# Kernel tuning notes

Hardware: AMD Instinct MI355X
Metric: run time of the kernel (lower is better)

Reference implementation:

```python
import jax, jax.numpy as jnp
import numpy as np

TOP_K = 2          # n_activated_experts
ROUTE_SCALE = 1.0  # args.route_scale


def setup_inputs() -> dict:
    key = jax.random.key(0)
    ks = jax.random.split(key, 12)
    B, S, D, I, E = 8, 2048, 512, 1024, 8
    SH = 2 * I  # n_shared_experts * moe_inter_dim
    std = 0.02
    return {
        "x": jax.random.normal(ks[0], (B, S, D), jnp.float32),
        "gate_w": (jax.random.normal(ks[1], (E, D), jnp.float32) * std),
        "w1": (jax.random.normal(ks[2], (E, D, I), jnp.float32) * std),
        "w2": (jax.random.normal(ks[3], (E, I, D), jnp.float32) * std),
        "w3": (jax.random.normal(ks[4], (E, D, I), jnp.float32) * std),
        "sw1": (jax.random.normal(ks[5], (D, SH), jnp.float32) * std),
        "sb1": jnp.zeros((SH,), jnp.float32),
        "sw2": (jax.random.normal(ks[6], (SH, D), jnp.float32) * std),
        "sb2": jnp.zeros((D,), jnp.float32),
        "sw3": (jax.random.normal(ks[7], (D, SH), jnp.float32) * std),
        "sb3": jnp.zeros((SH,), jnp.float32),
    }


def reference(x, gate_w, w1, w2, w3, sw1, sb1, sw2, sb2, sw3, sb3):
    B, S, D = x.shape
    xt = x.reshape(-1, D)              # [T, D] tokens
    T = xt.shape[0]
    E = gate_w.shape[0]

    # --- Gate: sigmoid scores, top-k, renormalized weights ---
    scores = jax.nn.sigmoid(xt @ gate_w.T)                 # [T, E]
    topv, topi = jax.lax.top_k(scores, TOP_K)              # [T, K]
    wts = topv / jnp.sum(topv, axis=-1, keepdims=True)
    wts = wts * ROUTE_SCALE

    # Dense combine weights: zero for non-selected experts -> faithful to
    # the torch masked scatter-accumulate over the expert loop.
    cw = jnp.zeros((T, E), xt.dtype).at[jnp.arange(T)[:, None], topi].add(wts)

    # --- Routed SwiGLU experts (ffn_bias=False) ---
    y = jnp.zeros_like(xt)
    for e in range(E):  # fixed small structural loop over experts
        h = jax.nn.silu(xt @ w1[e]) * (xt @ w3[e])         # [T, I]
        y = y + cw[:, e:e + 1] * (h @ w2[e])               # combine

    # --- Load-balance aux loss L_ExpBal ---
    counts = jnp.zeros((E,), xt.dtype).at[topi.reshape(-1)].add(1.0)
    f_i = E * counts / (TOP_K * T)
    P_i = cw.sum(axis=0) / T   # per-expert sum of routed weights
    L_ExpBal = jnp.sum(f_i * P_i)

    # --- Shared experts MLP (biased Linear, SwiGLU) ---
    z = (jax.nn.silu(xt @ sw1 + sb1) * (xt @ sw3 + sb3)) @ sw2 + sb2

    return (y + z).reshape(B, S, D), L_ExpBal
```

## Files before the change

kernel.cpp:

```cpp
#include <hip/hip_runtime.h>
#include <math.h>
#include <stdint.h>

#define T_TOK 16384
#define DDIM  512
#define IDIM  1024
#define NEXP  8
#define SHDIM 2048
#define MT_R  264
#define MPAD  (MT_R * 128)
#define GBLK  256

typedef unsigned short u16;
typedef short bf16x8 __attribute__((ext_vector_type(8)));
typedef float f32x4 __attribute__((ext_vector_type(4)));

__device__ __forceinline__ u16 f2bf(float f) {
    unsigned u = __float_as_uint(f);
    u += 0x7FFF + ((u >> 16) & 1);
    return (u16)(u >> 16);
}
__device__ __forceinline__ float bf2f(u16 h) {
    return __uint_as_float((unsigned)h << 16);
}

__device__ __forceinline__ void gload_lds16(const void* g, void* l) {
    __builtin_amdgcn_global_load_lds(
        (const __attribute__((address_space(1))) void*)g,
        (__attribute__((address_space(3))) void*)l, 16, 0, 0);
}

__device__ __forceinline__ int xcd_swz(int id, int nwg) {
    return (id & 7) * (nwg >> 3) + (id >> 3);
}

__device__ __forceinline__ int ksw(int r) { return (r >> 1) & 3; }

__global__ void k_zero(int* cursors) {
    int i = threadIdx.x;
    if (i < NEXP) cursors[i] = 0;
}

__global__ __launch_bounds__(256) void k_gate(
    const float* __restrict__ x, const float* __restrict__ gw,
    int* __restrict__ topi, float* __restrict__ wts,
    int* __restrict__ pcnt, float* __restrict__ pps, u16* __restrict__ xb)
{
    __shared__ int   cnt[NEXP];
    __shared__ float ps[NEXP];
    const int tid = threadIdx.x;
    if (tid < NEXP) { cnt[tid] = 0; ps[tid] = 0.f; }
    __syncthreads();
    const int wid = tid >> 6, lane = tid & 63;

    const float4* gw4 = (const float4*)gw;
    float4 g0[NEXP], g1[NEXP];
#pragma unroll
    for (int e = 0; e < NEXP; e++) {
        g0[e] = gw4[e * 128 + lane];
        g1[e] = gw4[e * 128 + 64 + lane];
    }

    const int t0 = blockIdx.x * 64 + wid * 16;
    for (int u = 0; u < 16; u++) {
        int t = t0 + u;
        const float4* xr4 = (const float4*)(x + (size_t)t * DDIM);
        float4 v0 = xr4[lane];
        float4 v1 = xr4[64 + lane];
        ushort4 o0 = { f2bf(v0.x), f2bf(v0.y), f2bf(v0.z), f2bf(v0.w) };
        ushort4 o1 = { f2bf(v1.x), f2bf(v1.y), f2bf(v1.z), f2bf(v1.w) };
        ushort4* xbo = (ushort4*)(xb + (size_t)t * DDIM);
        xbo[lane] = o0;
        xbo[64 + lane] = o1;
        float acc[NEXP];
#pragma unroll
        for (int e = 0; e < NEXP; e++) {
            acc[e] = v0.x * g0[e].x + v0.y * g0[e].y + v0.z * g0[e].z + v0.w * g0[e].w
                   + v1.x * g1[e].x + v1.y * g1[e].y + v1.z * g1[e].z + v1.w * g1[e].w;
        }
#pragma unroll
        for (int e = 0; e < NEXP; e++) {
#pragma unroll
            for (int off = 32; off; off >>= 1) acc[e] += __shfl_xor(acc[e], off, 64);
        }
        if (lane == 0) {
            float s[NEXP];
#pragma unroll
            for (int e = 0; e < NEXP; e++) s[e] = 1.f / (1.f + expf(-acc[e]));
            int i1 = 0; float v1s = s[0];
#pragma unroll
            for (int e = 1; e < NEXP; e++) if (s[e] > v1s) { v1s = s[e]; i1 = e; }
            int i2 = -1; float v2s = -1.f;
#pragma unroll
            for (int e = 0; e < NEXP; e++) if (e != i1 && s[e] > v2s) { v2s = s[e]; i2 = e; }
            float inv = 1.f / (v1s + v2s);
            float wa = v1s * inv, wb = v2s * inv;
            topi[2 * t] = i1; topi[2 * t + 1] = i2;
            wts[2 * t] = wa;  wts[2 * t + 1] = wb;
            atomicAdd(&cnt[i1], 1); atomicAdd(&cnt[i2], 1);
            atomicAdd(&ps[i1], wa); atomicAdd(&ps[i2], wb);
        }
    }
    __syncthreads();
    if (tid < NEXP) {
        pcnt[blockIdx.x * NEXP + tid] = cnt[tid];
        pps[blockIdx.x * NEXP + tid]  = ps[tid];
    }
}

__global__ void k_scan(const int* __restrict__ pcnt, const float* __restrict__ pps,
                       int* __restrict__ off_pad, float* __restrict__ out_loss)
{
    __shared__ int   scnt[8][NEXP];
    __shared__ float sps[8][NEXP];
    int tid = threadIdx.x;
    if (tid < 64) {
        int e = tid & 7, part = tid >> 3;
        int c = 0; float p = 0.f;
        for (int b = part * 32; b < part * 32 + 32; b++) {
            c += pcnt[b * NEXP + e];
            p += pps[b * NEXP + e];
        }
        scnt[part][e] = c; sps[part][e] = p;
    }
    __syncthreads();
    if (tid == 0) {
        int off = 0; float L = 0.f;
        for (int e = 0; e < NEXP; e++) {
            int c = 0; float p = 0.f;
            for (int q = 0; q < 8; q++) { c += scnt[q][e]; p += sps[q][e]; }
            off_pad[e] = off;
            off += (c + 127) & ~127;
            float f = (float)NEXP * (float)c / (float)(2 * T_TOK);
            L += f * (p / (float)T_TOK);
        }
        off_pad[NEXP] = off;
        out_loss[0] = L;
    }
}

__global__ void k_fillperm(int* __restrict__ perm, u16* __restrict__ zpad) {
    int i = blockIdx.x * blockDim.x + threadIdx.x;
    if (i < MPAD) perm[i] = -1;
    if (blockIdx.x == 0 && threadIdx.x < 256) ((unsigned*)zpad)[threadIdx.x] = 0u;
}

__global__ __launch_bounds__(256) void k_scatter(
    const int* __restrict__ topi, const float* __restrict__ wts,
    const int* __restrict__ off_pad, int* __restrict__ cursors,
    int* __restrict__ perm, float* __restrict__ pw, int* __restrict__ inv)
{
    __shared__ int lcnt[NEXP];
    __shared__ int lbase[NEXP];
    int tid = threadIdx.x;
    if (tid < NEXP) lcnt[tid] = 0;
    __syncthreads();
    int t = blockIdx.x * 256 + tid;
    int e0 = topi[2 * t], e1 = topi[2 * t + 1];
    int p0 = atomicAdd(&lcnt[e0], 1);
    int p1 = atomicAdd(&lcnt[e1], 1);
    __syncthreads();
    if (tid < NEXP) lbase[tid] = atomicAdd(&cursors[tid], lcnt[tid]);
    __syncthreads();
    int s0 = off_pad[e0] + lbase[e0] + p0;
    int s1 = off_pad[e1] + lbase[e1] + p1;
    perm[s0] = t; pw[s0] = wts[2 * t];
    perm[s1] = t; pw[s1] = wts[2 * t + 1];
    inv[2 * t] = s0; inv[2 * t + 1] = s1;
}

__global__ __launch_bounds__(256) void k_transpose(const float* __restrict__ src,
                                                   u16* __restrict__ dst, int R, int C)
{
    __shared__ u16 t[64][68];
    const float* s = src + (size_t)blockIdx.z * R * C;
    u16* d = dst + (size_t)blockIdx.z * R * C;
    int r0 = blockIdx.y * 64, c0 = blockIdx.x * 64;
    int tid = threadIdx.x;
    int lr = tid >> 4, lc = (tid & 15) * 4;
#pragma unroll
    for (int u = 0; u < 4; u++) {
        int r = lr + u * 16;
        float4 v = *(const float4*)&s[(size_t)(r0 + r) * C + c0 + lc];
        t[lc + 0][r] = f2bf(v.x);
        t[lc + 1][r] = f2bf(v.y);
        t[lc + 2][r] = f2bf(v.z);
        t[lc + 3][r] = f2bf(v.w);
    }
    __syncthreads();
    int wr = tid >> 4, wc = (tid & 15) * 4;
#pragma unroll
    for (int u = 0; u < 4; u++) {
        int c = wr + u * 16;
        ushort4 o = { t[c][wc], t[c][wc + 1], t[c][wc + 2], t[c][wc + 3] };
        *(ushort4*)&d[(size_t)(c0 + c) * R + r0 + wc] = o;
    }
}

template<bool ROUTED, bool BIAS>
__global__ __launch_bounds__(256, 3) void k_s1(
    const u16* __restrict__ Axb, const u16* __restrict__ B1t, const u16* __restrict__ B3t,
    const float* __restrict__ bias1, const float* __restrict__ bias3,
    u16* __restrict__ H, int ldh, const int* __restrict__ off_pad,
    const int* __restrict__ perm, const u16* __restrict__ zpad)
{
    __shared__ __align__(16) unsigned char smem[3 * 16384];
    const int nwg = gridDim.x * gridDim.y;
    const int id  = xcd_swz(blockIdx.y * gridDim.x + blockIdx.x, nwg);
    const int m0 = (id / gridDim.x) * 128;
    const int n0 = (id % gridDim.x) * 64;
    if (ROUTED && m0 >= off_pad[NEXP]) return;
    const u16* b1 = B1t; const u16* b3 = B3t;
    if (ROUTED) {
        int e = 0;
        while (off_pad[e + 1] <= m0) e++;
        b1 += (size_t)e * IDIM * DDIM;
        b3 += (size_t)e * IDIM * DDIM;
    }
    const int tid = threadIdx.x;
    const int wid = tid >> 6, lane = tid & 63;
    const int fr = lane & 15, hi = lane >> 4;
    const int wrow = (wid >> 1) * 64, wcol = (wid & 1) * 32;

    const u16* ap[2]; const u16* b1p; const u16* b3p;
    int dstA[2];
#pragma unroll
    for (int s = 0; s < 2; s++) {
        int r = s * 64 + (tid >> 2);
        int goff = ((tid & 3) ^ ksw(r)) * 8;
        dstA[s] = s * 4096 + tid * 16;
        if (ROUTED) {
            int tok = perm[m0 + r];
            ap[s] = (tok >= 0 ? Axb + (size_t)tok * DDIM : zpad) + goff;
        } else {
            ap[s] = Axb + (size_t)(m0 + r) * DDIM + goff;
        }
    }
    {
        int rb = tid >> 2;
        int goffb = ((tid & 3) ^ ksw(rb)) * 8;
        b1p = b1 + (size_t)(n0 + rb) * DDIM + goffb;
        b3p = b3 + (size_t)(n0 + rb) * DDIM + goffb;
    }
    const int dstB = tid * 16;

    int aoff[4], boff[2];
#pragma unroll
    for (int i = 0; i < 4; i++) {
        int ar = wrow + i * 16 + fr;
        aoff[i] = ar * 64 + ((hi ^ ksw(ar)) << 4);
    }
#pragma unroll
    for (int j = 0; j < 2; j++) {
        int br = wcol + j * 16 + fr;
        boff[j] = br * 64 + ((hi ^ ksw(br)) << 4);
    }

    f32x4 acc1[4][2], acc3[4][2];
#pragma unroll
    for (int i = 0; i < 4; i++)
#pragma unroll
        for (int j = 0; j < 2; j++) { acc1[i][j] = {0.f, 0.f, 0.f, 0.f}; acc3[i][j] = {0.f, 0.f, 0.f, 0.f}; }

    const int NT = DDIM / 32;
#pragma unroll
    for (int t = 0; t < 2; t++) {
        unsigned char* bb = smem + t * 16384;
        gload_lds16(ap[0] + t * 32, bb + dstA[0]);
        gload_lds16(ap[1] + t * 32, bb + dstA[1]);
        gload_lds16(b1p   + t * 32, bb + 8192  + dstB);
        gload_lds16(b3p   + t * 32, bb + 12288 + dstB);
    }

    int bufc = 0;
    for (int t = 0; t < NT; t++) {
        int bufn = bufc + 2; if (bufn >= 3) bufn -= 3;
        if (t + 2 < NT) {
            unsigned char* bb = smem + bufn * 16384;
            int k2 = (t + 2) * 32;
            gload_lds16(ap[0] + k2, bb + dstA[0]);
            gload_lds16(ap[1] + k2, bb + dstA[1]);
            gload_lds16(b1p   + k2, bb + 8192  + dstB);
            gload_lds16(b3p   + k2, bb + 12288 + dstB);
            asm volatile("s_waitcnt vmcnt(8)" ::: "memory");
        } else if (t + 2 == NT) {
            asm volatile("s_waitcnt vmcnt(4)" ::: "memory");
        } else {
            asm volatile("s_waitcnt vmcnt(0)" ::: "memory");
        }
        __builtin_amdgcn_s_barrier();
        __builtin_amdgcn_sched_barrier(0);
        const unsigned char* cb = smem + bufc * 16384;
        bf16x8 av[4], b1v[2], b3v[2];
#pragma unroll
        for (int i = 0; i < 4; i++) av[i] = *(const bf16x8*)(cb + aoff[i]);
#pragma unroll
        for (int j = 0; j < 2; j++) {
            b1v[j] = *(const bf16x8*)(cb + 8192  + boff[j]);
            b3v[j] = *(const bf16x8*)(cb + 12288 + boff[j]);
        }
        __builtin_amdgcn_s_setprio(1);
#pragma unroll
        for (int i = 0; i < 4; i++)
#pragma unroll
            for (int j = 0; j < 2; j++) {
                acc1[i][j] = __builtin_amdgcn_mfma_f32_16x16x32_bf16(av[i], b1v[j], acc1[i][j], 0, 0, 0);
                acc3[i][j] = __builtin_amdgcn_mfma_f32_16x16x32_bf16(av[i], b3v[j], acc3[i][j], 0, 0, 0);
            }
        __builtin_amdgcn_s_setprio(0);
        __builtin_amdgcn_sched_barrier(0);
        __builtin_amdgcn_s_barrier();
        bufc++; if (bufc >= 3) bufc -= 3;
    }

    const int rr = hi * 4;
#pragma unroll
    for (int i = 0; i < 4; i++) {
#pragma unroll
        for (int j = 0; j < 2; j++) {
            int col = n0 + wcol + j * 16 + fr;
            float bb1 = BIAS ? bias1[col] : 0.f;
            float bb3 = BIAS ? bias3[col] : 0.f;
#pragma unroll
            for (int r = 0; r < 4; r++) {
                int row = m0 + wrow + i * 16 + rr + r;
                float v1 = acc1[i][j][r] + bb1;
                float v3 = acc3[i][j][r] + bb3;
                float hv = (v1 / (1.f + __expf(-v1))) * v3;
                H[(size_t)row * ldh + col] = f2bf(hv);
            }
        }
    }
}

template<int K, bool ROUTED>
__global__ __launch_bounds__(256, 3) void k_s2(
    const u16* __restrict__ A, const u16* __restrict__ Bt,
    const float* __restrict__ bias2, float* __restrict__ out,
    u16* __restrict__ ytmp, const int* __restrict__ off_pad)
{
    __shared__ __align__(16) unsigned char smem[3 * 16384];
    const int nwg = gridDim.x * gridDim.y;
    const int id  = xcd_swz(blockIdx.y * gridDim.x + blockIdx.x, nwg);
    const int m0 = (id / gridDim.x) * 128;
    const int n0 = (id % gridDim.x) * 128;
    if (ROUTED && m0 >= off_pad[NEXP]) return;
    const u16* bt = Bt;
    if (ROUTED) {
        int e = 0;
        while (off_pad[e + 1] <= m0) e++;
        bt += (size_t)e * DDIM * IDIM;
    }
    const int tid = threadIdx.x;
    const int wid = tid >> 6, lane = tid & 63;
    const int fr = lane & 15, hi = lane >> 4;
    const int wrow = (wid >> 1) * 64, wcol = (wid & 1) * 64;

    const u16* ap[2]; const u16* bp[2];
    int dst_[2];
#pragma unroll
    for (int s = 0; s < 2; s++) {
        int r = s * 64 + (tid >> 2);
        int goff = ((tid & 3) ^ ksw(r)) * 8;
        dst_[s] = s * 4096 + tid * 16;
        ap[s] = A  + (size_t)(m0 + r) * K + goff;
        bp[s] = bt + (size_t)(n0 + r) * K + goff;
    }
    int aoff[4], boff[4];
#pragma unroll
    for (int i = 0; i < 4; i++) {
        int ar = wrow + i * 16 + fr;
        aoff[i] = ar * 64 + ((hi ^ ksw(ar)) << 4);
        int br = wcol + i * 16 + fr;
        boff[i] = br * 64 + ((hi ^ ksw(br)) << 4);
    }

    f32x4 acc[4][4];
#pragma unroll
    for (int i = 0; i < 4; i++)
#pragma unroll
        for (int j = 0; j < 4; j++) acc[i][j] = {0.f, 0.f, 0.f, 0.f};

    const int NT = K / 32;
#pragma unroll
    for (int t = 0; t < 2; t++) {
        unsigned char* bb = smem + t * 16384;
#pragma unroll
        for (int s = 0; s < 2; s++) {
            gload_lds16(ap[s] + t * 32, bb + dst_[s]);
            gload_lds16(bp[s] + t * 32, bb + 8192 + dst_[s]);
        }
    }

    int bufc = 0;
    for (int t = 0; t < NT; t++) {
        int bufn = bufc + 2; if (bufn >= 3) bufn -= 3;
        if (t + 2 < NT) {
            unsigned char* bb = smem + bufn * 16384;
            int k2 = (t + 2) * 32;
#pragma unroll
            for (int s = 0; s < 2; s++) {
                gload_lds16(ap[s] + k2, bb + dst_[s]);
                gload_lds16(bp[s] + k2, bb + 8192 + dst_[s]);
            }
            asm volatile("s_waitcnt vmcnt(8)" ::: "memory");
        } else if (t + 2 == NT) {
            asm volatile("s_waitcnt vmcnt(4)" ::: "memory");
        } else {
            asm volatile("s_waitcnt vmcnt(0)" ::: "memory");
        }
        __builtin_amdgcn_s_barrier();
        __builtin_amdgcn_sched_barrier(0);
        const unsigned char* cb = smem + bufc * 16384;
        bf16x8 av[4], bv[4];
#pragma unroll
        for (int i = 0; i < 4; i++) {
            av[i] = *(const bf16x8*)(cb + aoff[i]);
            bv[i] = *(const bf16x8*)(cb + 8192 + boff[i]);
        }
        __builtin_amdgcn_s_setprio(1);
#pragma unroll
        for (int i = 0; i < 4; i++)
#pragma unroll
            for (int j = 0; j < 4; j++)
                acc[i][j] = __builtin_amdgcn_mfma_f32_16x16x32_bf16(av[i], bv[j], acc[i][j], 0, 0, 0);
        __builtin_amdgcn_s_setprio(0);
        __builtin_amdgcn_sched_barrier(0);
        __builtin_amdgcn_s_barrier();
        bufc++; if (bufc >= 3) bufc -= 3;
    }

    const int rr = hi * 4;
#pragma unroll
    for (int i = 0; i < 4; i++) {
#pragma unroll
        for (int r = 0; r < 4; r++) {
            int row = m0 + wrow + i * 16 + rr + r;
#pragma unroll
            for (int j = 0; j < 4; j++) {
                int col = n0 + wcol + j * 16 + fr;
                float v = acc[i][j][r];
                if (ROUTED) {
                    ytmp[(size_t)row * DDIM + col] = f2bf(v);
                } else {
                    out[(size_t)row * DDIM + col] = v + bias2[col];
                }
            }
        }
    }
}

__global__ __launch_bounds__(256) void k_combine(
    const u16* __restrict__ ytmp, const int* __restrict__ inv,
    const float* __restrict__ wts, float* __restrict__ out)
{
    int idx = blockIdx.x * 256 + threadIdx.x;
    int t = idx >> 7;
    int c = (idx & 127) * 4;
    int s0 = inv[2 * t], s1 = inv[2 * t + 1];
    float w0 = wts[2 * t], w1 = wts[2 * t + 1];
    ushort4 a = *(const ushort4*)&ytmp[(size_t)s0 * DDIM + c];
    ushort4 b = *(const ushort4*)&ytmp[(size_t)s1 * DDIM + c];
    float4 o = *(float4*)&out[(size_t)t * DDIM + c];
    o.x += w0 * bf2f(a.x) + w1 * bf2f(b.x);
    o.y += w0 * bf2f(a.y) + w1 * bf2f(b.y);
    o.z += w0 * bf2f(a.z) + w1 * bf2f(b.z);
    o.w += w0 * bf2f(a.w) + w1 * bf2f(b.w);
    *(float4*)&out[(size_t)t * DDIM + c] = o;
}

extern "C" void kernel_launch(void* const* d_in, const int* in_sizes, int n_in,
                              void* d_out, int out_size, void* d_ws, size_t ws_size,
                              hipStream_t stream)
{
    const float* x   = (const float*)d_in[0];
    const float* gw  = (const float*)d_in[1];
    const float* w1  = (const float*)d_in[2];
    const float* w2  = (const float*)d_in[3];
    const float* w3  = (const float*)d_in[4];
    const float* sw1 = (const float*)d_in[5];
    const float* sb1 = (const float*)d_in[6];
    const float* sw2 = (const float*)d_in[7];
    const float* sb2 = (const float*)d_in[8];
    const float* sw3 = (const float*)d_in[9];
    const float* sb3 = (const float*)d_in[10];
    float* out = (float*)d_out;

    char* ws = (char*)d_ws;
    size_t off = 0;
    int*   topi    = (int*)(ws + off);   off += (size_t)2 * T_TOK * 4;
    float* wts     = (float*)(ws + off); off += (size_t)2 * T_TOK * 4;
    int*   perm    = (int*)(ws + off);   off += (size_t)MPAD * 4;
    float* pw      = (float*)(ws + off); off += (size_t)MPAD * 4;
    int*   cursors = (int*)(ws + off);   off += 256;
    int*   off_pad = (int*)(ws + off);   off += 256;
    int*   pcnt    = (int*)(ws + off);   off += (size_t)GBLK * NEXP * 4;
    float* pps     = (float*)(ws + off); off += (size_t)GBLK * NEXP * 4;
    int*   inv     = (int*)(ws + off);   off += (size_t)2 * T_TOK * 4;
    u16*   zpad    = (u16*)(ws + off);   off += 1024;
    u16*   xb      = (u16*)(ws + off);   off += (size_t)T_TOK * DDIM * 2;
    u16*   ytmp    = (u16*)(ws + off);   off += (size_t)MPAD * DDIM * 2;
    u16*   w1T     = (u16*)(ws + off);   off += (size_t)NEXP * IDIM * DDIM * 2;
    u16*   w3T     = (u16*)(ws + off);   off += (size_t)NEXP * IDIM * DDIM * 2;
    u16*   w2T     = (u16*)(ws + off);   off += (size_t)NEXP * DDIM * IDIM * 2;
    u16*   sw1T    = (u16*)(ws + off);   off += (size_t)SHDIM * DDIM * 2;
    u16*   sw3T    = (u16*)(ws + off);   off += (size_t)SHDIM * DDIM * 2;
    u16*   sw2T    = (u16*)(ws + off);   off += (size_t)DDIM * SHDIM * 2;
    u16*   hb      = (u16*)(ws + off);   off += (size_t)MPAD * IDIM * 2;

    k_zero<<<1, 64, 0, stream>>>(cursors);
    k_gate<<<GBLK, 256, 0, stream>>>(x, gw, topi, wts, pcnt, pps, xb);
    k_scan<<<1, 64, 0, stream>>>(pcnt, pps, off_pad, out + (size_t)T_TOK * DDIM);
    k_fillperm<<<MPAD / 256, 256, 0, stream>>>(perm, zpad);
    k_scatter<<<T_TOK / 256, 256, 0, stream>>>(topi, wts, off_pad, cursors, perm, pw, inv);

    k_transpose<<<dim3(IDIM / 64, DDIM / 64, NEXP), 256, 0, stream>>>(w1, w1T, DDIM, IDIM);
    k_transpose<<<dim3(IDIM / 64, DDIM / 64, NEXP), 256, 0, stream>>>(w3, w3T, DDIM, IDIM);
    k_transpose<<<dim3(DDIM / 64, IDIM / 64, NEXP), 256, 0, stream>>>(w2, w2T, IDIM, DDIM);
    k_transpose<<<dim3(SHDIM / 64, DDIM / 64, 1), 256, 0, stream>>>(sw1, sw1T, DDIM, SHDIM);
    k_transpose<<<dim3(SHDIM / 64, DDIM / 64, 1), 256, 0, stream>>>(sw3, sw3T, DDIM, SHDIM);
    k_transpose<<<dim3(DDIM / 64, SHDIM / 64, 1), 256, 0, stream>>>(sw2, sw2T, SHDIM, DDIM);

    k_s1<false, true><<<dim3(SHDIM / 64, T_TOK / 128), 256, 0, stream>>>(
        xb, sw1T, sw3T, sb1, sb3, hb, SHDIM, nullptr, nullptr, nullptr);
    k_s2<SHDIM, false><<<dim3(DDIM / 128, T_TOK / 128), 256, 0, stream>>>(
        hb, sw2T, sb2, out, nullptr, nullptr);
    k_s1<true, false><<<dim3(IDIM / 64, MT_R), 256, 0, stream>>>(
        xb, w1T, w3T, nullptr, nullptr, hb, IDIM, off_pad, perm, zpad);
    k_s2<IDIM, true><<<dim3(DDIM / 128, MT_R), 256, 0, stream>>>(
        hb, w2T, nullptr, nullptr, ytmp, off_pad);
    k_combine<<<(T_TOK * DDIM / 4) / 256, 256, 0, stream>>>(ytmp, inv, wts, out);
}
```

Baseline: 355.8 us.

## Make GEMM kernels persistent with cross-tile prefetch and per-XCD job partitioning

Converts the four GEMM kernels from one-tile-per-block grids to persistent kernels with a fixed grid of 768 blocks. Each XCD gets a contiguous range of tile jobs, and the first k-slices of the next tile are prefetched into LDS while the current tile finishes. For the routed experts, only the tiles that are actually populated are distributed, instead of launching the padded maximum and early-exiting. A separate zero-init kernel launch is also folded into the scan kernel. The cost is extra register pressure and more control logic in the main loop.

```diff
diff --git a/kernel.cpp b/kernel.cpp
--- a/kernel.cpp
+++ b/kernel.cpp
@@ -10,6 +10,8 @@
 #define MT_R  264
 #define MPAD  (MT_R * 128)
 #define GBLK  256
+#define NB    768
+#define BPX   96
 
 typedef unsigned short u16;
 typedef short bf16x8 __attribute__((ext_vector_type(8)));
@@ -30,16 +32,7 @@
         (__attribute__((address_space(3))) void*)l, 16, 0, 0);
 }
 
-__device__ __forceinline__ int xcd_swz(int id, int nwg) {
-    return (id & 7) * (nwg >> 3) + (id >> 3);
-}
-
 __device__ __forceinline__ int ksw(int r) { return (r >> 1) & 3; }
-
-__global__ void k_zero(int* cursors) {
-    int i = threadIdx.x;
-    if (i < NEXP) cursors[i] = 0;
-}
 
 __global__ __launch_bounds__(256) void k_gate(
     const float* __restrict__ x, const float* __restrict__ gw,
@@ -109,11 +102,13 @@
 }
 
 __global__ void k_scan(const int* __restrict__ pcnt, const float* __restrict__ pps,
-                       int* __restrict__ off_pad, float* __restrict__ out_loss)
+                       int* __restrict__ off_pad, float* __restrict__ out_loss,
+                       int* __restrict__ cursors)
 {
     __shared__ int   scnt[8][NEXP];
     __shared__ float sps[8][NEXP];
     int tid = threadIdx.x;
+    if (tid < NEXP) cursors[tid] = 0;
     if (tid < 64) {
         int e = tid & 7, part = tid >> 3;
         int c = 0; float p = 0.f;
@@ -197,52 +192,59 @@
     }
 }
 
-template<bool ROUTED, bool BIAS>
+struct S1Src { const u16 *a0, *a1, *b1, *b3; int m0, n0; };
+struct S2Src { const u16 *a0, *a1, *b0, *b1; int m0, n0; };
+
+template<bool ROUTED>
+__device__ __forceinline__ S1Src s1_build(
+    int m0, int n0, int tk0, int tk1, int r0, int g0,
+    const u16* Axb, const u16* B1t, const u16* B3t,
+    const int* opad, const u16* zpad)
+{
+    S1Src s; s.m0 = m0; s.n0 = n0;
+    const u16* b1 = B1t; const u16* b3 = B3t;
+    if (ROUTED) {
+        int e = 0;
+#pragma unroll
+        for (int k = 1; k < NEXP; k++) e += (opad[k] <= m0) ? 1 : 0;
+        b1 += (size_t)e * IDIM * DDIM;
+        b3 += (size_t)e * IDIM * DDIM;
+        s.a0 = (tk0 >= 0 ? Axb + (size_t)tk0 * DDIM : zpad) + g0;
+        s.a1 = (tk1 >= 0 ? Axb + (size_t)tk1 * DDIM : zpad) + g0;
+    } else {
+        s.a0 = Axb + (size_t)(m0 + r0) * DDIM + g0;
+        s.a1 = Axb + (size_t)(m0 + 64 + r0) * DDIM + g0;
+    }
+    s.b1 = b1 + (size_t)(n0 + r0) * DDIM + g0;
+    s.b3 = b3 + (size_t)(n0 + r0) * DDIM + g0;
+    return s;
+}
+
+template<bool ROUTED, bool BIAS, int GX>
 __global__ __launch_bounds__(256, 3) void k_s1(
     const u16* __restrict__ Axb, const u16* __restrict__ B1t, const u16* __restrict__ B3t,
     const float* __restrict__ bias1, const float* __restrict__ bias3,
     u16* __restrict__ H, int ldh, const int* __restrict__ off_pad,
-    const int* __restrict__ perm, const u16* __restrict__ zpad)
+    const int* __restrict__ perm, const u16* __restrict__ zpad, int njobs_s)
 {
     __shared__ __align__(16) unsigned char smem[3 * 16384];
-    const int nwg = gridDim.x * gridDim.y;
-    const int id  = xcd_swz(blockIdx.y * gridDim.x + blockIdx.x, nwg);
-    const int m0 = (id / gridDim.x) * 128;
-    const int n0 = (id % gridDim.x) * 64;
-    if (ROUTED && m0 >= off_pad[NEXP]) return;
-    const u16* b1 = B1t; const u16* b3 = B3t;
-    if (ROUTED) {
-        int e = 0;
-        while (off_pad[e + 1] <= m0) e++;
-        b1 += (size_t)e * IDIM * DDIM;
-        b3 += (size_t)e * IDIM * DDIM;
-    }
+    int opad[NEXP + 1];
+#pragma unroll
+    for (int k = 0; k <= NEXP; k++) opad[k] = ROUTED ? off_pad[k] : 0;
+    const int njobs = ROUTED ? ((opad[NEXP] >> 7) * GX) : njobs_s;
+    const int b = blockIdx.x, xcd = b & 7, bx = b >> 3;
+    const int q = njobs >> 3, r8 = njobs & 7;
+    const int base = xcd < r8 ? xcd * (q + 1) : r8 * (q + 1) + (xcd - r8) * q;
+    const int cnt = q + (xcd < r8 ? 1 : 0);
+    if (bx >= cnt) return;
+
     const int tid = threadIdx.x;
     const int wid = tid >> 6, lane = tid & 63;
     const int fr = lane & 15, hi = lane >> 4;
     const int wrow = (wid >> 1) * 64, wcol = (wid & 1) * 32;
-
-    const u16* ap[2]; const u16* b1p; const u16* b3p;
-    int dstA[2];
-#pragma unroll
-    for (int s = 0; s < 2; s++) {
-        int r = s * 64 + (tid >> 2);
-        int goff = ((tid & 3) ^ ksw(r)) * 8;
-        dstA[s] = s * 4096 + tid * 16;
-        if (ROUTED) {
-            int tok = perm[m0 + r];
-            ap[s] = (tok >= 0 ? Axb + (size_t)tok * DDIM : zpad) + goff;
-        } else {
-            ap[s] = Axb + (size_t)(m0 + r) * DDIM + goff;
-        }
-    }
-    {
-        int rb = tid >> 2;
-        int goffb = ((tid & 3) ^ ksw(rb)) * 8;
-        b1p = b1 + (size_t)(n0 + rb) * DDIM + goffb;
-        b3p = b3 + (size_t)(n0 + rb) * DDIM + goffb;
-    }
-    const int dstB = tid * 16;
+    const int r0 = tid >> 2;
+    const int g0 = ((tid & 3) ^ ksw(r0)) * 8;
+    const int dstT = tid * 16;
 
     int aoff[4], boff[2];
 #pragma unroll
@@ -256,6 +258,13 @@
         boff[j] = br * 64 + ((hi ^ ksw(br)) << 4);
     }
 
+#define S1_STAGE(S, kk, bb) do { \
+        gload_lds16((S).a0 + (kk), (bb) + dstT); \
+        gload_lds16((S).a1 + (kk), (bb) + 4096 + dstT); \
+        gload_lds16((S).b1 + (kk), (bb) + 8192 + dstT); \
+        gload_lds16((S).b3 + (kk), (bb) + 12288 + dstT); \
+    } while (0)
+
     f32x4 acc1[4][2], acc3[4][2];
 #pragma unroll
     for (int i = 0; i < 4; i++)
@@ -263,109 +272,122 @@
         for (int j = 0; j < 2; j++) { acc1[i][j] = {0.f, 0.f, 0.f, 0.f}; acc3[i][j] = {0.f, 0.f, 0.f, 0.f}; }
 
     const int NT = DDIM / 32;
-#pragma unroll
-    for (int t = 0; t < 2; t++) {
-        unsigned char* bb = smem + t * 16384;
-        gload_lds16(ap[0] + t * 32, bb + dstA[0]);
-        gload_lds16(ap[1] + t * 32, bb + dstA[1]);
-        gload_lds16(b1p   + t * 32, bb + 8192  + dstB);
-        gload_lds16(b3p   + t * 32, bb + 12288 + dstB);
-    }
+
+    int lj = bx;
+    int j0 = base + lj;
+    int m0c = (j0 / GX) * 128, n0c = (j0 % GX) * 64;
+    int tk0 = 0, tk1 = 0;
+    if (ROUTED) { tk0 = perm[m0c + r0]; tk1 = perm[m0c + 64 + r0]; }
+    S1Src cur = s1_build<ROUTED>(m0c, n0c, tk0, tk1, r0, g0, Axb, B1t, B3t, opad, zpad);
+    S1_STAGE(cur, 0, smem);
+    S1_STAGE(cur, 32, smem + 16384);
 
     int bufc = 0;
-    for (int t = 0; t < NT; t++) {
-        int bufn = bufc + 2; if (bufn >= 3) bufn -= 3;
-        if (t + 2 < NT) {
+    while (true) {
+        const bool hn = (lj + BPX) < cnt;
+        int m0n = 0, n0n = 0, ntk0 = 0, ntk1 = 0;
+        if (hn) {
+            int jn = base + lj + BPX;
+            m0n = (jn / GX) * 128; n0n = (jn % GX) * 64;
+            if (ROUTED) { ntk0 = perm[m0n + r0]; ntk1 = perm[m0n + 64 + r0]; }
+        }
+        S1Src nxt;
+        for (int t = 0; t < NT; t++) {
+            int bufn = bufc + 2; if (bufn >= 3) bufn -= 3;
             unsigned char* bb = smem + bufn * 16384;
-            int k2 = (t + 2) * 32;
-            gload_lds16(ap[0] + k2, bb + dstA[0]);
-            gload_lds16(ap[1] + k2, bb + dstA[1]);
-            gload_lds16(b1p   + k2, bb + 8192  + dstB);
-            gload_lds16(b3p   + k2, bb + 12288 + dstB);
-            asm volatile("s_waitcnt vmcnt(8)" ::: "memory");
-        } else if (t + 2 == NT) {
-            asm volatile("s_waitcnt vmcnt(4)" ::: "memory");
-        } else {
-            asm volatile("s_waitcnt vmcnt(0)" ::: "memory");
-        }
-        __builtin_amdgcn_s_barrier();
-        __builtin_amdgcn_sched_barrier(0);
-        const unsigned char* cb = smem + bufc * 16384;
-        bf16x8 av[4], b1v[2], b3v[2];
-#pragma unroll
-        for (int i = 0; i < 4; i++) av[i] = *(const bf16x8*)(cb + aoff[i]);
-#pragma unroll
-        for (int j = 0; j < 2; j++) {
-            b1v[j] = *(const bf16x8*)(cb + 8192  + boff[j]);
-            b3v[j] = *(const bf16x8*)(cb + 12288 + boff[j]);
-        }
-        __builtin_amdgcn_s_setprio(1);
+            if (t + 2 < NT) {
+                S1_STAGE(cur, (t + 2) * 32, bb);
+                asm volatile("s_waitcnt vmcnt(8)" ::: "memory");
+            } else if (hn) {
+                if (t + 2 == NT)
+                    nxt = s1_build<ROUTED>(m0n, n0n, ntk0, ntk1, r0, g0, Axb, B1t, B3t, opad, zpad);
+                S1_STAGE(nxt, (t + 2 - NT) * 32, bb);
+                asm volatile("s_waitcnt vmcnt(8)" ::: "memory");
+            } else if (t + 2 == NT) {
+                asm volatile("s_waitcnt vmcnt(4)" ::: "memory");
+            } else {
+                asm volatile("s_waitcnt vmcnt(0)" ::: "memory");
+            }
+            __builtin_amdgcn_s_barrier();
+            __builtin_amdgcn_sched_barrier(0);
+            const unsigned char* cb = smem + bufc * 16384;
+            bf16x8 av[4], b1v[2], b3v[2];
+#pragma unroll
+            for (int i = 0; i < 4; i++) av[i] = *(const bf16x8*)(cb + aoff[i]);
+#pragma unroll
+            for (int j = 0; j < 2; j++) {
+                b1v[j] = *(const bf16x8*)(cb + 8192  + boff[j]);
+                b3v[j] = *(const bf16x8*)(cb + 12288 + boff[j]);
+            }
+            __builtin_amdgcn_s_setprio(1);
+#pragma unroll
+            for (int i = 0; i < 4; i++)
+#pragma unroll
+                for (int j = 0; j < 2; j++) {
+                    acc1[i][j] = __builtin_amdgcn_mfma_f32_16x16x32_bf16(av[i], b1v[j], acc1[i][j], 0, 0, 0);
+                    acc3[i][j] = __builtin_amdgcn_mfma_f32_16x16x32_bf16(av[i], b3v[j], acc3[i][j], 0, 0, 0);
+                }
+            __builtin_amdgcn_s_setprio(0);
+            __builtin_amdgcn_sched_barrier(0);
+            __builtin_amdgcn_s_barrier();
+            bufc++; if (bufc >= 3) bufc -= 3;
+        }
+
+        const int rr = hi * 4;
+#pragma unroll
+        for (int i = 0; i < 4; i++) {
+#pragma unroll
+            for (int j = 0; j < 2; j++) {
+                int col = cur.n0 + wcol + j * 16 + fr;
+                float bb1 = BIAS ? bias1[col] : 0.f;
+                float bb3 = BIAS ? bias3[col] : 0.f;
+#pragma unroll
+                for (int r = 0; r < 4; r++) {
+                    int row = cur.m0 + wrow + i * 16 + rr + r;
+                    float v1 = acc1[i][j][r] + bb1;
+                    float v3 = acc3[i][j][r] + bb3;
+                    float hv = (v1 / (1.f + __expf(-v1))) * v3;
+                    H[(size_t)row * ldh + col] = f2bf(hv);
+                }
+            }
+        }
+        if (!hn) break;
 #pragma unroll
         for (int i = 0; i < 4; i++)
 #pragma unroll
-            for (int j = 0; j < 2; j++) {
-                acc1[i][j] = __builtin_amdgcn_mfma_f32_16x16x32_bf16(av[i], b1v[j], acc1[i][j], 0, 0, 0);
-                acc3[i][j] = __builtin_amdgcn_mfma_f32_16x16x32_bf16(av[i], b3v[j], acc3[i][j], 0, 0, 0);
-            }
-        __builtin_amdgcn_s_setprio(0);
-        __builtin_amdgcn_sched_barrier(0);
-        __builtin_amdgcn_s_barrier();
-        bufc++; if (bufc >= 3) bufc -= 3;
-    }
-
-    const int rr = hi * 4;
-#pragma unroll
-    for (int i = 0; i < 4; i++) {
-#pragma unroll
-        for (int j = 0; j < 2; j++) {
-            int col = n0 + wcol + j * 16 + fr;
-            float bb1 = BIAS ? bias1[col] : 0.f;
-            float bb3 = BIAS ? bias3[col] : 0.f;
-#pragma unroll
-            for (int r = 0; r < 4; r++) {
-                int row = m0 + wrow + i * 16 + rr + r;
-                float v1 = acc1[i][j][r] + bb1;
-                float v3 = acc3[i][j][r] + bb3;
-                float hv = (v1 / (1.f + __expf(-v1))) * v3;
-                H[(size_t)row * ldh + col] = f2bf(hv);
-            }
-        }
-    }
-}
-
-template<int K, bool ROUTED>
+            for (int j = 0; j < 2; j++) { acc1[i][j] = {0.f, 0.f, 0.f, 0.f}; acc3[i][j] = {0.f, 0.f, 0.f, 0.f}; }
+        cur = nxt;
+        lj += BPX;
+    }
+#undef S1_STAGE
+}
+
+template<int K, int EPI, int GX>
 __global__ __launch_bounds__(256, 3) void k_s2(
     const u16* __restrict__ A, const u16* __restrict__ Bt,
     const float* __restrict__ bias2, float* __restrict__ out,
-    u16* __restrict__ ytmp, const int* __restrict__ off_pad)
-{
+    u16* __restrict__ ytmp, const int* __restrict__ off_pad, int njobs_s)
+{
+    constexpr bool ROUTED = (EPI == 2);
     __shared__ __align__(16) unsigned char smem[3 * 16384];
-    const int nwg = gridDim.x * gridDim.y;
-    const int id  = xcd_swz(blockIdx.y * gridDim.x + blockIdx.x, nwg);
-    const int m0 = (id / gridDim.x) * 128;
-    const int n0 = (id % gridDim.x) * 128;
-    if (ROUTED && m0 >= off_pad[NEXP]) return;
-    const u16* bt = Bt;
-    if (ROUTED) {
-        int e = 0;
-        while (off_pad[e + 1] <= m0) e++;
-        bt += (size_t)e * DDIM * IDIM;
-    }
+    int opad[NEXP + 1];
+#pragma unroll
+    for (int k = 0; k <= NEXP; k++) opad[k] = ROUTED ? off_pad[k] : 0;
+    const int njobs = ROUTED ? ((opad[NEXP] >> 7) * GX) : njobs_s;
+    const int b = blockIdx.x, xcd = b & 7, bx = b >> 3;
+    const int q = njobs >> 3, r8 = njobs & 7;
+    const int base = xcd < r8 ? xcd * (q + 1) : r8 * (q + 1) + (xcd - r8) * q;
+    const int cnt = q + (xcd < r8 ? 1 : 0);
+    if (bx >= cnt) return;
+
     const int tid = threadIdx.x;
     const int wid = tid >> 6, lane = tid & 63;
     const int fr = lane & 15, hi = lane >> 4;
     const int wrow = (wid >> 1) * 64, wcol = (wid & 1) * 64;
-
-    const u16* ap[2]; const u16* bp[2];
-    int dst_[2];
-#pragma unroll
-    for (int s = 0; s < 2; s++) {
-        int r = s * 64 + (tid >> 2);
-        int goff = ((tid & 3) ^ ksw(r)) * 8;
-        dst_[s] = s * 4096 + tid * 16;
-        ap[s] = A  + (size_t)(m0 + r) * K + goff;
-        bp[s] = bt + (size_t)(n0 + r) * K + goff;
-    }
+    const int r0 = tid >> 2;
+    const int g0 = ((tid & 3) ^ ksw(r0)) * 8;
+    const int dstT = tid * 16;
+
     int aoff[4], boff[4];
 #pragma unroll
     for (int i = 0; i < 4; i++) {
@@ -375,6 +397,29 @@
         boff[i] = br * 64 + ((hi ^ ksw(br)) << 4);
     }
 
+    auto build = [&](int m0, int n0) {
+        S2Src s; s.m0 = m0; s.n0 = n0;
+        const u16* bt = Bt;
+        if (ROUTED) {
+            int e = 0;
+#pragma unroll
+            for (int k = 1; k < NEXP; k++) e += (opad[k] <= m0) ? 1 : 0;
+            bt += (size_t)e * DDIM * IDIM;
+        }
+        s.a0 = A  + (size_t)(m0 + r0) * K + g0;
+        s.a1 = A  + (size_t)(m0 + 64 + r0) * K + g0;
+        s.b0 = bt + (size_t)(n0 + r0) * K + g0;
+        s.b1 = bt + (size_t)(n0 + 64 + r0) * K + g0;
+        return s;
+    };
+
+#define S2_STAGE(S, kk, bb) do { \
+        gload_lds16((S).a0 + (kk), (bb) + dstT); \
+        gload_lds16((S).a1 + (kk), (bb) + 4096 + dstT); \
+        gload_lds16((S).b0 + (kk), (bb) + 8192 + dstT); \
+        gload_lds16((S).b1 + (kk), (bb) + 12288 + dstT); \
+    } while (0)
+
     f32x4 acc[4][4];
 #pragma unroll
     for (int i = 0; i < 4; i++)
@@ -382,72 +427,82 @@
         for (int j = 0; j < 4; j++) acc[i][j] = {0.f, 0.f, 0.f, 0.f};
 
     const int NT = K / 32;
-#pragma unroll
-    for (int t = 0; t < 2; t++) {
-        unsigned char* bb = smem + t * 16384;
-#pragma unroll
-        for (int s = 0; s < 2; s++) {
-            gload_lds16(ap[s] + t * 32, bb + dst_[s]);
-            gload_lds16(bp[s] + t * 32, bb + 8192 + dst_[s]);
-        }
-    }
+
+    int lj = bx;
+    int j0 = base + lj;
+    S2Src cur = build((j0 / GX) * 128, (j0 % GX) * 128);
+    S2_STAGE(cur, 0, smem);
+    S2_STAGE(cur, 32, smem + 16384);
 
     int bufc = 0;
-    for (int t = 0; t < NT; t++) {
-        int bufn = bufc + 2; if (bufn >= 3) bufn -= 3;
-        if (t + 2 < NT) {
+    while (true) {
+        const bool hn = (lj + BPX) < cnt;
+        int m0n = 0, n0n = 0;
+        if (hn) {
+            int jn = base + lj + BPX;
+            m0n = (jn / GX) * 128; n0n = (jn % GX) * 128;
+        }
+        S2Src nxt;
+        for (int t = 0; t < NT; t++) {
+            int bufn = bufc + 2; if (bufn >= 3) bufn -= 3;
             unsigned char* bb = smem + bufn * 16384;
-            int k2 = (t + 2) * 32;
-#pragma unroll
-            for (int s = 0; s < 2; s++) {
-                gload_lds16(ap[s] + k2, bb + dst_[s]);
-                gload_lds16(bp[s] + k2, bb + 8192 + dst_[s]);
+            if (t + 2 < NT) {
+                S2_STAGE(cur, (t + 2) * 32, bb);
+                asm volatile("s_waitcnt vmcnt(8)" ::: "memory");
+            } else if (hn) {
+                if (t + 2 == NT) nxt = build(m0n, n0n);
+                S2_STAGE(nxt, (t + 2 - NT) * 32, bb);
+                asm volatile("s_waitcnt vmcnt(8)" ::: "memory");
+            } else if (t + 2 == NT) {
+                asm volatile("s_waitcnt vmcnt(4)" ::: "memory");
+            } else {
+                asm volatile("s_waitcnt vmcnt(0)" ::: "memory");
             }
-            asm volatile("s_waitcnt vmcnt(8)" ::: "memory");
-        } else if (t + 2 == NT) {
-            asm volatile("s_waitcnt vmcnt(4)" ::: "memory");
-        } else {
-            asm volatile("s_waitcnt vmcnt(0)" ::: "memory");
-        }
-        __builtin_amdgcn_s_barrier();
-        __builtin_amdgcn_sched_barrier(0);
-        const unsigned char* cb = smem + bufc * 16384;
-        bf16x8 av[4], bv[4];
+            __builtin_amdgcn_s_barrier();
+            __builtin_amdgcn_sched_barrier(0);
+            const unsigned char* cb = smem + bufc * 16384;
+            bf16x8 av[4], bv[4];
+#pragma unroll
+            for (int i = 0; i < 4; i++) {
+                av[i] = *(const bf16x8*)(cb + aoff[i]);
+                bv[i] = *(const bf16x8*)(cb + 8192 + boff[i]);
+            }
+            __builtin_amdgcn_s_setprio(1);
+#pragma unroll
+            for (int i = 0; i < 4; i++)
+#pragma unroll
+                for (int j = 0; j < 4; j++)
+                    acc[i][j] = __builtin_amdgcn_mfma_f32_16x16x32_bf16(av[i], bv[j], acc[i][j], 0, 0, 0);
+            __builtin_amdgcn_s_setprio(0);
+            __builtin_amdgcn_sched_barrier(0);
+            __builtin_amdgcn_s_barrier();
+            bufc++; if (bufc >= 3) bufc -= 3;
+        }
+
+        const int rr = hi * 4;
 #pragma unroll
         for (int i = 0; i < 4; i++) {
-            av[i] = *(const bf16x8*)(cb + aoff[i]);
-            bv[i] = *(const bf16x8*)(cb + 8192 + boff[i]);
-        }
-        __builtin_amdgcn_s_setprio(1);
-#pragma unroll
-        for (int i = 0; i < 4; i++)
-#pragma unroll
-            for (int j = 0; j < 4; j++)
-                acc[i][j] = __builtin_amdgcn_mfma_f32_16x16x32_bf16(av[i], bv[j], acc[i][j], 0, 0, 0);
-        __builtin_amdgcn_s_setprio(0);
-        __builtin_amdgcn_sched_barrier(0);
-        __builtin_amdgcn_s_barrier();
-        bufc++; if (bufc >= 3) bufc -= 3;
-    }
-
-    const int rr = hi * 4;
-#pragma unroll
-    for (int i = 0; i < 4; i++) {
-#pragma unroll
-        for (int r = 0; r < 4; r++) {
-            int row = m0 + wrow + i * 16 + rr + r;
-#pragma unroll
-            for (int j = 0; j < 4; j++) {
-                int col = n0 + wcol + j * 16 + fr;
-                float v = acc[i][j][r];
-                if (ROUTED) {
-                    ytmp[(size_t)row * DDIM + col] = f2bf(v);
-                } else {
-                    out[(size_t)row * DDIM + col] = v + bias2[col];
+#pragma unroll
+            for (int r = 0; r < 4; r++) {
+                int row = cur.m0 + wrow + i * 16 + rr + r;
+#pragma unroll
+                for (int j = 0; j < 4; j++) {
+                    int col = cur.n0 + wcol + j * 16 + fr;
+                    float v = acc[i][j][r];
+                    if (EPI == 2) ytmp[(size_t)row * DDIM + col] = f2bf(v);
+                    else          out[(size_t)row * DDIM + col] = v + bias2[col];
                 }
             }
         }
-    }
+        if (!hn) break;
+#pragma unroll
+        for (int i = 0; i < 4; i++)
+#pragma unroll
+            for (int j = 0; j < 4; j++) acc[i][j] = {0.f, 0.f, 0.f, 0.f};
+        cur = nxt;
+        lj += BPX;
+    }
+#undef S2_STAGE
 }
 
 __global__ __launch_bounds__(256) void k_combine(
@@ -508,9 +563,8 @@
     u16*   sw2T    = (u16*)(ws + off);   off += (size_t)DDIM * SHDIM * 2;
     u16*   hb      = (u16*)(ws + off);   off += (size_t)MPAD * IDIM * 2;
 
-    k_zero<<<1, 64, 0, stream>>>(cursors);
     k_gate<<<GBLK, 256, 0, stream>>>(x, gw, topi, wts, pcnt, pps, xb);
-    k_scan<<<1, 64, 0, stream>>>(pcnt, pps, off_pad, out + (size_t)T_TOK * DDIM);
+    k_scan<<<1, 64, 0, stream>>>(pcnt, pps, off_pad, out + (size_t)T_TOK * DDIM, cursors);
     k_fillperm<<<MPAD / 256, 256, 0, stream>>>(perm, zpad);
     k_scatter<<<T_TOK / 256, 256, 0, stream>>>(topi, wts, off_pad, cursors, perm, pw, inv);
 
@@ -521,13 +575,14 @@
     k_transpose<<<dim3(SHDIM / 64, DDIM / 64, 1), 256, 0, stream>>>(sw3, sw3T, DDIM, SHDIM);
     k_transpose<<<dim3(DDIM / 64, SHDIM / 64, 1), 256, 0, stream>>>(sw2, sw2T, SHDIM, DDIM);
 
-    k_s1<false, true><<<dim3(SHDIM / 64, T_TOK / 128), 256, 0, stream>>>(
-        xb, sw1T, sw3T, sb1, sb3, hb, SHDIM, nullptr, nullptr, nullptr);
-    k_s2<SHDIM, false><<<dim3(DDIM / 128, T_TOK / 128), 256, 0, stream>>>(
-        hb, sw2T, sb2, out, nullptr, nullptr);
-    k_s1<true, false><<<dim3(IDIM / 64, MT_R), 256, 0, stream>>>(
-        xb, w1T, w3T, nullptr, nullptr, hb, IDIM, off_pad, perm, zpad);
-    k_s2<IDIM, true><<<dim3(DDIM / 128, MT_R), 256, 0, stream>>>(
-        hb, w2T, nullptr, nullptr, ytmp, off_pad);
+    k_s1<false, true, SHDIM / 64><<<NB, 256, 0, stream>>>(
+        xb, sw1T, sw3T, sb1, sb3, hb, SHDIM, off_pad, nullptr, nullptr,
+        (T_TOK / 128) * (SHDIM / 64));
+    k_s2<SHDIM, 1, DDIM / 128><<<NB, 256, 0, stream>>>(
+        hb, sw2T, sb2, out, nullptr, off_pad, (T_TOK / 128) * (DDIM / 128));
+    k_s1<true, false, IDIM / 64><<<NB, 256, 0, stream>>>(
+        xb, w1T, w3T, nullptr, nullptr, hb, IDIM, off_pad, perm, zpad, 0);
+    k_s2<IDIM, 2, DDIM / 128><<<NB, 256, 0, stream>>>(
+        hb, w2T, nullptr, nullptr, ytmp, off_pad, 0);
     k_combine<<<(T_TOK * DDIM / 4) / 256, 256, 0, stream>>>(ytmp, inv, wts, out);
 }
```

New measurement: 359.8 us. Within noise of the previous version (+1.1%).
